# Performance work log

Hardware: AMD Instinct MI355X
Metric: run time of the kernel (lower is better)

Reference implementation:

```python
import jax, jax.numpy as jnp
import numpy as np

OUT = 7          # roi_align output_size
NUM_ANCHORS = 27 # 3 scales x 3 ratios x 3 angles
MAX_PROPOSALS = 100
RPN_STRIDE = 32


def conv2d(x, w, b, stride=1, pad=1):
    y = jax.lax.conv_general_dilated(
        x, w, (stride, stride), [(pad, pad), (pad, pad)],
        dimension_numbers=('NCHW', 'OIHW', 'NCHW'))
    return y + b[None, :, None, None]


def generate_anchors(H, W, stride):
    # matches CustomOrientedRPN.generate_anchors
    sx = np.arange(0, W * stride, stride, dtype=np.float32)
    sy = np.arange(0, H * stride, stride, dtype=np.float32)
    SY, SX = np.meshgrid(sy, sx, indexing='ij')
    shifts = np.stack([SX, SY], axis=-1).reshape(-1, 2)  # [HW,2]
    base = []
    for scale in (32.0, 64.0, 128.0):
        for ratio in (0.5, 1.0, 2.0):
            w = scale * ratio ** 0.5
            h = scale / ratio ** 0.5
            for angle in (0.0, 45.0, 90.0):
                base.append([w, h, angle])
    base = np.array(base, dtype=np.float32)  # [A,3]
    A = base.shape[0]
    anchors = np.concatenate(
        [np.repeat(shifts[:, None, :], A, axis=1),
         np.broadcast_to(base[None], (shifts.shape[0], A, 3))], axis=-1)
    return jnp.asarray(anchors.reshape(-1, 5))  # [HW*A, 5]


def rotated_roi_align(features, boxes, batch_idx):
    # Vectorized version of the per-box affine_grid + grid_sample loop
    # (align_corners=False semantics for both, zero padding for grid_sample).
    B, C, Hf, Wf = features.shape
    lin = (2.0 * jnp.arange(OUT, dtype=features.dtype) + 1.0) / OUT - 1.0
    ys, xs = jnp.meshgrid(lin, lin, indexing='ij')  # [7,7] base grid

    cx, cy, w, h, ang = (boxes[:, i] for i in range(5))
    ar = -ang * jnp.pi / 180.0
    c, s = jnp.cos(ar), jnp.sin(ar)
    t00 = w / Wf * c; t01 = -h / Hf * s; t02 = 2.0 * cx / Wf - 1.0
    t10 = w / Wf * s; t11 = h / Hf * c;  t12 = 2.0 * cy / Hf - 1.0
    gx = t00[:, None, None] * xs + t01[:, None, None] * ys + t02[:, None, None]  # [N,7,7]
    gy = t10[:, None, None] * xs + t11[:, None, None] * ys + t12[:, None, None]

    ix = ((gx + 1.0) * Wf - 1.0) / 2.0
    iy = ((gy + 1.0) * Hf - 1.0) / 2.0
    x0 = jnp.floor(ix); y0 = jnp.floor(iy)
    wx = ix - x0;       wy = iy - y0
    x0i = x0.astype(jnp.int32); y0i = y0.astype(jnp.int32)

    def gather(dx, dy, wgt):
        xi = x0i + dx; yi = y0i + dy
        valid = (xi >= 0) & (xi < Wf) & (yi >= 0) & (yi < Hf)
        xc = jnp.clip(xi, 0, Wf - 1)
        yc = jnp.clip(yi, 0, Hf - 1)
        def one(bi, yb, xb):
            return features[bi][:, yb, xb]  # [C,7,7]
        vals = jax.vmap(one)(batch_idx, yc, xc)  # [N,C,7,7]
        return vals * (wgt * valid)[:, None, :, :]

    return (gather(0, 0, (1 - wx) * (1 - wy)) + gather(1, 0, wx * (1 - wy)) +
            gather(0, 1, (1 - wx) * wy) + gather(1, 1, wx * wy))


def setup_inputs() -> dict:
    key = jax.random.key(0)
    ks = jax.random.split(key, 20)

    def w(k, shape):
        fan_in = int(np.prod(shape[1:]))
        return jax.random.normal(k, shape, jnp.float32) / np.sqrt(fan_in)

    C = 256; A = NUM_ANCHORS; NC = 5
    return {
        'images': jax.random.normal(ks[0], (8, 3, 1024, 1024), jnp.float32),
        'backbone_w': w(ks[1], (C, 3, 3, 3)),   'backbone_b': jnp.zeros((C,), jnp.float32),
        'rpn_conv_w': w(ks[2], (256, C, 3, 3)), 'rpn_conv_b': jnp.zeros((256,), jnp.float32),
        'obj_w': w(ks[3], (A, 256, 1, 1)),      'obj_b': jnp.zeros((A,), jnp.float32),
        'delta_w': w(ks[4], (A * 5, 256, 1, 1)) * 0.1, 'delta_b': jnp.zeros((A * 5,), jnp.float32),
        'fc1_w': w(ks[5], (1024, C * OUT * OUT)), 'fc1_b': jnp.zeros((1024,), jnp.float32),
        'fc2_w': w(ks[6], (1024, 1024)),          'fc2_b': jnp.zeros((1024,), jnp.float32),
        'cls_w': w(ks[7], (NC, 1024)),            'cls_b': jnp.zeros((NC,), jnp.float32),
        'bbox_w': w(ks[8], (5, 1024)),            'bbox_b': jnp.zeros((5,), jnp.float32),
    }


def reference(images, backbone_w, backbone_b, rpn_conv_w, rpn_conv_b,
              obj_w, obj_b, delta_w, delta_b,
              fc1_w, fc1_b, fc2_w, fc2_b, cls_w, cls_b, bbox_w, bbox_b):
    # backbone (stand-in: single stride-16 conv)
    f = conv2d(images, backbone_w, backbone_b, stride=16, pad=1)  # [B,256,64,64]
    B, C, H, W = f.shape
    # F.interpolate(scale_factor=0.5, bilinear, align_corners=False) == 2x2 mean
    f = f.reshape(B, C, H // 2, 2, W // 2, 2).mean(axis=(3, 5))   # [B,256,32,32]
    Hf, Wf = f.shape[2], f.shape[3]

    # RPN
    t = jax.nn.relu(conv2d(f, rpn_conv_w, rpn_conv_b, 1, 1))
    _logits = conv2d(t, obj_w, obj_b, 1, 0)  # computed as in original (unused downstream)
    deltas = conv2d(t, delta_w, delta_b, 1, 0)  # [B, A*5, Hf, Wf]
    A = NUM_ANCHORS
    deltas = deltas.reshape(B, A, 5, Hf, Wf).transpose(0, 3, 4, 1, 2).reshape(B, -1, 5)

    anchors = generate_anchors(Hf, Wf, RPN_STRIDE)  # [HW*A,5]
    acx, acy, aw, ah, aa = (anchors[:, i] for i in range(5))
    pcx = deltas[:, :, 0] * aw + acx
    pcy = deltas[:, :, 1] * ah + acy
    pw = jnp.exp(deltas[:, :, 2]) * aw
    ph = jnp.exp(deltas[:, :, 3]) * ah
    pa = aa + deltas[:, :, 4]
    proposals = jnp.stack([pcx, pcy, pw, ph, pa], axis=-1)  # [B, HW*A, 5]
    proposals = proposals[:, :MAX_PROPOSALS]                # p[:max_proposals]

    boxes = proposals.reshape(-1, 5)                        # [B*100, 5]
    batch_idx = jnp.repeat(jnp.arange(B), MAX_PROPOSALS)
    pooled = rotated_roi_align(f, boxes, batch_idx)         # [B*100, 256, 7, 7]

    x = pooled.reshape(pooled.shape[0], -1)
    x = jax.nn.relu(x @ fc1_w.T + fc1_b)
    x = jax.nn.relu(x @ fc2_w.T + fc2_b)
    class_logits = x @ cls_w.T + cls_b
    obb_preds = x @ bbox_w.T + bbox_b
    return class_logits, obb_preds
```

## Files before the change

### kernel.cpp

```cpp
#include <hip/hip_runtime.h>
#include <hip/hip_bf16.h>

using bf16 = __hip_bfloat16;

typedef __attribute__((ext_vector_type(8))) short bf16x8;
typedef __attribute__((ext_vector_type(4))) float f32x4;

__device__ __forceinline__ void async16(const void* g, void* l) {
  __builtin_amdgcn_global_load_lds(
      (const __attribute__((address_space(1))) unsigned int*)g,
      (__attribute__((address_space(3))) unsigned int*)l, 16, 0, 0);
}

__device__ __forceinline__ void store_o(float* C, size_t i, float v) { C[i] = v; }
__device__ __forceinline__ void store_o(bf16* C, size_t i, float v) {
  C[i] = __float2bfloat16(v);
}

__global__ __launch_bounds__(256) void k_backbone(const float* __restrict__ img,
    const float* __restrict__ w, const float* __restrict__ bias,
    float* __restrict__ f) {
  int blk = blockIdx.x;
  int x = blk & 31, y = (blk >> 5) & 31, b = blk >> 10;
  __shared__ float patch[4 * 27];
  int t = threadIdx.x;
  if (t < 108) {
    int kx = t % 3, ky = (t / 3) % 3, cin = (t / 9) % 3, sub = t / 27;
    int sy = sub >> 1, sx = sub & 1;
    int iy = (2 * y + sy) * 16 - 1 + ky;
    int ix = (2 * x + sx) * 16 - 1 + kx;
    float v = 0.f;
    if (iy >= 0 && ix >= 0)
      v = img[((size_t)(b * 3 + cin) * 1024 + iy) * 1024 + ix];
    patch[t] = v;
  }
  __syncthreads();
  int c = t;
  float wr[27];
#pragma unroll
  for (int k = 0; k < 27; ++k) wr[k] = w[c * 27 + k];
  float acc = 0.f;
#pragma unroll
  for (int sub = 0; sub < 4; ++sub)
#pragma unroll
    for (int k = 0; k < 27; ++k)
      acc += patch[sub * 27 + k] * wr[k];
  f[(size_t)blk * 256 + c] = acc * 0.25f + bias[c];
}

__global__ __launch_bounds__(256) void k_rpn(const float* __restrict__ f,
    const float* __restrict__ rpn_w, float* __restrict__ part) {
  int p = blockIdx.x;
  int kc = blockIdx.y;
  int x = p & 3, b = p >> 2;
  __shared__ float fpl[6][16];
  int tid = threadIdx.x;
  if (tid < 96) {
    int cin2 = tid & 15;
    int rc = tid >> 4;
    int row = rc / 3, col = rc % 3;
    int xc = x - 1 + col;
    float v = 0.f;
    if (xc >= 0)
      v = f[((size_t)(b * 32 + row) * 32 + xc) * 256 + kc * 16 + cin2];
    fpl[rc][cin2] = v;
  }
  __syncthreads();
  int c = tid;
  const float* wbase = rpn_w + (size_t)c * 2304 + kc * 144;
  float acc = 0.f;
#pragma unroll
  for (int cin2 = 0; cin2 < 16; ++cin2) {
    const float* wp = wbase + cin2 * 9;
    acc += fpl[0][cin2] * wp[3] + fpl[1][cin2] * wp[4]
         + fpl[2][cin2] * wp[5] + fpl[3][cin2] * wp[6]
         + fpl[4][cin2] * wp[7] + fpl[5][cin2] * wp[8];
  }
  part[((size_t)kc * 32 + p) * 256 + c] = acc;
}

__global__ __launch_bounds__(512) void k_delta(const float* __restrict__ part,
    const float* __restrict__ rpn_b,
    const float* __restrict__ dw, const float* __restrict__ db,
    float* __restrict__ boxes) {
  int p = blockIdx.x;
  int x = p & 3, b = p >> 2;
  __shared__ float tbuf[256];
  __shared__ float dvals[135];
  int tid = threadIdx.x;
  if (tid < 256) {
    float s = rpn_b[tid];
#pragma unroll
    for (int kc = 0; kc < 16; ++kc)
      s += part[((size_t)kc * 32 + p) * 256 + tid];
    tbuf[tid] = fmaxf(s, 0.f);
  }
  __syncthreads();
  if (tid < 270) {
    int o = tid >> 1, half = tid & 1;
    const float* wp = dw + (size_t)o * 256 + half * 128;
    const float* tp = tbuf + half * 128;
    float s = 0.f;
#pragma unroll 8
    for (int k = 0; k < 128; ++k) s += tp[k] * wp[k];
    s += __shfl_xor(s, 1, 64);
    if (half == 0) dvals[o] = s + db[o];
  }
  __syncthreads();
  if (tid < 27) {
    int i = x * 27 + tid;
    if (i < 100) {
      int a = tid;
      int si = a / 9, ri = (a / 3) % 3, ai = a % 3;
      float scale = 32.f * (float)(1 << si);
      float sr = (ri == 0) ? 0.70710678118654752f : (ri == 1 ? 1.0f : 1.41421356237309505f);
      float aw = scale * sr, ah = scale / sr;
      float aang = 45.f * (float)ai;
      float acx = 32.f * (float)x, acy = 0.f;
      float* bx = boxes + (size_t)(b * 100 + i) * 5;
      bx[0] = dvals[a * 5 + 0] * aw + acx;
      bx[1] = dvals[a * 5 + 1] * ah + acy;
      bx[2] = expf(dvals[a * 5 + 2]) * aw;
      bx[3] = expf(dvals[a * 5 + 3]) * ah;
      bx[4] = aang + dvals[a * 5 + 4];
    }
  }
}

__global__ __launch_bounds__(256) void k_roialign(const float* __restrict__ f,
    const float* __restrict__ boxes, bf16* __restrict__ pooled) {
  int n = blockIdx.x;
  int b = n / 100;
  __shared__ int six[49], siy[49];
  __shared__ float swx[49], swy[49];
  __shared__ float pool_s[12544];
  int tid = threadIdx.x;
  if (tid < 49) {
    float cx = boxes[n * 5 + 0], cy = boxes[n * 5 + 1];
    float w = boxes[n * 5 + 2], h = boxes[n * 5 + 3], ang = boxes[n * 5 + 4];
    float ar = -ang * 0.017453292519943295f;
    float cc = cosf(ar), ss = sinf(ar);
    float t00 = w * (1.f / 32.f) * cc, t01 = -h * (1.f / 32.f) * ss;
    float t02 = cx * (2.f / 32.f) - 1.f;
    float t10 = w * (1.f / 32.f) * ss, t11 = h * (1.f / 32.f) * cc;
    float t12 = cy * (2.f / 32.f) - 1.f;
    int py = tid / 7, px = tid - py * 7;
    float lx = (2.f * px + 1.f) * (1.f / 7.f) - 1.f;
    float ly = (2.f * py + 1.f) * (1.f / 7.f) - 1.f;
    float gx = t00 * lx + t01 * ly + t02;
    float gy = t10 * lx + t11 * ly + t12;
    float ix = ((gx + 1.f) * 32.f - 1.f) * 0.5f;
    float iy = ((gy + 1.f) * 32.f - 1.f) * 0.5f;
    float x0 = floorf(ix), y0 = floorf(iy);
    six[tid] = (int)x0; siy[tid] = (int)y0;
    swx[tid] = ix - x0; swy[tid] = iy - y0;
  }
  __syncthreads();
  const float* fb = f + (size_t)b * 262144;
  int c = tid;
  for (int bin = 0; bin < 49; ++bin) {
    int x0 = six[bin], y0 = siy[bin];
    float wx = swx[bin], wy = swy[bin];
    float acc = 0.f;
    if (x0 >= 0 && x0 < 32 && y0 >= 0 && y0 < 32)
      acc += fb[(y0 * 32 + x0) * 256 + c] * ((1.f - wx) * (1.f - wy));
    if (x0 + 1 >= 0 && x0 + 1 < 32 && y0 >= 0 && y0 < 32)
      acc += fb[(y0 * 32 + x0 + 1) * 256 + c] * (wx * (1.f - wy));
    if (x0 >= 0 && x0 < 32 && y0 + 1 >= 0 && y0 + 1 < 32)
      acc += fb[((y0 + 1) * 32 + x0) * 256 + c] * ((1.f - wx) * wy);
    if (x0 + 1 >= 0 && x0 + 1 < 32 && y0 + 1 >= 0 && y0 + 1 < 32)
      acc += fb[((y0 + 1) * 32 + x0 + 1) * 256 + c] * (wx * wy);
    pool_s[c * 49 + bin] = acc;
  }
  __syncthreads();
  bf16* po = pooled + (size_t)n * 12544;
  for (int k = tid; k < 12544; k += 256) po[k] = __float2bfloat16(pool_s[k]);
}

__global__ __launch_bounds__(256) void k_gemm_sk(
    const unsigned short* __restrict__ A, const float* __restrict__ B,
    float* __restrict__ P, int M, int N, int K, int KC) {
  __shared__ unsigned short As[128 * 64];
  __shared__ unsigned short Bs[64 * 72];
  int t = threadIdx.x;
  int wv = t >> 6, ln = t & 63;
  int quad = ln >> 4, l15 = ln & 15;
  int wm = wv >> 1, wn = wv & 1;
  int n0 = blockIdx.x * 64, m0 = blockIdx.y * 128;
  int kbeg = blockIdx.z * KC;
  int kend = kbeg + KC; if (kend > K) kend = K;

  int srow = ln >> 3;
  int sg = (ln & 7) ^ srow;
  const unsigned short* Ap[4];
#pragma unroll
  for (int q = 0; q < 4; ++q) {
    int r = m0 + q * 32 + wv * 8 + srow;
    if (r > M - 1) r = M - 1;
    Ap[q] = A + (size_t)r * K + sg * 8;
  }

  int brow = t >> 2, bq = t & 3;
  const float* Bp = B + (size_t)(n0 + brow) * K + bq * 16;
  unsigned short* bdst = &Bs[brow * 72 + bq * 16];

  f32x4 acc[4][2];
#pragma unroll
  for (int mf = 0; mf < 4; ++mf)
#pragma unroll
    for (int nf = 0; nf < 2; ++nf) acc[mf][nf] = (f32x4){0.f, 0.f, 0.f, 0.f};

  for (int k0 = kbeg; k0 < kend; k0 += 64) {
    float4 bv0 = *(const float4*)(Bp + k0);
    float4 bv1 = *(const float4*)(Bp + k0 + 4);
    float4 bv2 = *(const float4*)(Bp + k0 + 8);
    float4 bv3 = *(const float4*)(Bp + k0 + 12);
    __syncthreads();
#pragma unroll
    for (int q = 0; q < 4; ++q)
      async16(Ap[q] + k0, &As[q * 2048 + wv * 512]);
    unsigned short bb[16];
    bb[0]  = __bfloat16_as_ushort(__float2bfloat16(bv0.x));
    bb[1]  = __bfloat16_as_ushort(__float2bfloat16(bv0.y));
    bb[2]  = __bfloat16_as_ushort(__float2bfloat16(bv0.z));
    bb[3]  = __bfloat16_as_ushort(__float2bfloat16(bv0.w));
    bb[4]  = __bfloat16_as_ushort(__float2bfloat16(bv1.x));
    bb[5]  = __bfloat16_as_ushort(__float2bfloat16(bv1.y));
    bb[6]  = __bfloat16_as_ushort(__float2bfloat16(bv1.z));
    bb[7]  = __bfloat16_as_ushort(__float2bfloat16(bv1.w));
    bb[8]  = __bfloat16_as_ushort(__float2bfloat16(bv2.x));
    bb[9]  = __bfloat16_as_ushort(__float2bfloat16(bv2.y));
    bb[10] = __bfloat16_as_ushort(__float2bfloat16(bv2.z));
    bb[11] = __bfloat16_as_ushort(__float2bfloat16(bv2.w));
    bb[12] = __bfloat16_as_ushort(__float2bfloat16(bv3.x));
    bb[13] = __bfloat16_as_ushort(__float2bfloat16(bv3.y));
    bb[14] = __bfloat16_as_ushort(__float2bfloat16(bv3.z));
    bb[15] = __bfloat16_as_ushort(__float2bfloat16(bv3.w));
#pragma unroll
    for (int u = 0; u < 2; ++u)
      *(bf16x8*)(bdst + u * 8) = *(const bf16x8*)(bb + u * 8);
    __syncthreads();
#pragma unroll
    for (int ks = 0; ks < 2; ++ks) {
      bf16x8 a[4];
#pragma unroll
      for (int mf = 0; mf < 4; ++mf) {
        int row = wm * 64 + mf * 16 + l15;
        a[mf] = *(const bf16x8*)&As[row * 64 + (((ks * 4 + quad) ^ (l15 & 7)) * 8)];
      }
#pragma unroll
      for (int nf = 0; nf < 2; ++nf) {
        bf16x8 b = *(const bf16x8*)&Bs[(wn * 32 + nf * 16 + l15) * 72 + ks * 32 + quad * 8];
#pragma unroll
        for (int mf = 0; mf < 4; ++mf)
          acc[mf][nf] = __builtin_amdgcn_mfma_f32_16x16x32_bf16(a[mf], b, acc[mf][nf], 0, 0, 0);
      }
    }
  }
#pragma unroll
  for (int nf = 0; nf < 2; ++nf) {
    int n = n0 + wn * 32 + nf * 16 + l15;
#pragma unroll
    for (int mf = 0; mf < 4; ++mf) {
#pragma unroll
      for (int r = 0; r < 4; ++r) {
        int m = m0 + wm * 64 + mf * 16 + quad * 4 + r;
        if (m < M) atomicAdd(&P[(size_t)m * N + n], acc[mf][nf][r]);
      }
    }
  }
}

template <typename OutT>
__global__ __launch_bounds__(256) void k_bias_relu(const float* __restrict__ P,
    const float* __restrict__ bias, OutT* __restrict__ C, int MN, int N) {
  int i = blockIdx.x * 256 + threadIdx.x;
  if (i * 4 >= MN) return;
  f32x4 s = *(const f32x4*)(P + (size_t)i * 4);
  int n = (i * 4) % N;
#pragma unroll
  for (int u = 0; u < 4; ++u)
    store_o(C, (size_t)i * 4 + u, fmaxf(s[u] + bias[n + u], 0.f));
}

__global__ __launch_bounds__(640) void k_heads(const float* __restrict__ x2,
    const float* __restrict__ cls_w, const float* __restrict__ cls_b,
    const float* __restrict__ bbox_w, const float* __restrict__ bbox_b,
    float* __restrict__ out) {
  int n = blockIdx.x;
  int wave = threadIdx.x >> 6;
  int lane = threadIdx.x & 63;
  const float* w = (wave < 5) ? (cls_w + (size_t)wave * 1024)
                              : (bbox_w + (size_t)(wave - 5) * 1024);
  const float* xr = x2 + (size_t)n * 1024;
  float s = 0.f;
  for (int k = lane; k < 1024; k += 64) s += xr[k] * w[k];
  for (int off = 32; off; off >>= 1) s += __shfl_down(s, off, 64);
  if (lane == 0) {
    int o = (wave < 5) ? wave : wave - 5;
    float bias = (wave < 5) ? cls_b[o] : bbox_b[o];
    int base = (wave < 5) ? 0 : 4000;
    out[base + n * 5 + o] = s + bias;
  }
}

extern "C" void kernel_launch(void* const* d_in, const int* in_sizes, int n_in,
                              void* d_out, int out_size, void* d_ws, size_t ws_size,
                              hipStream_t stream) {
  const float* images     = (const float*)d_in[0];
  const float* backbone_w = (const float*)d_in[1];
  const float* backbone_b = (const float*)d_in[2];
  const float* rpn_w      = (const float*)d_in[3];
  const float* rpn_b      = (const float*)d_in[4];
  const float* delta_w    = (const float*)d_in[7];
  const float* delta_b    = (const float*)d_in[8];
  const float* fc1_w      = (const float*)d_in[9];
  const float* fc1_b      = (const float*)d_in[10];
  const float* fc2_w      = (const float*)d_in[11];
  const float* fc2_b      = (const float*)d_in[12];
  const float* cls_w      = (const float*)d_in[13];
  const float* cls_b      = (const float*)d_in[14];
  const float* bbox_w     = (const float*)d_in[15];
  const float* bbox_b     = (const float*)d_in[16];

  char* ws = (char*)d_ws;
  float* f      = (float*)ws;
  float* boxes  = (float*)(ws + 8388608);
  bf16*  pooled = (bf16*) (ws + 8404992);
  bf16*  x1     = (bf16*) (ws + 28475392);
  float* x2     = (float*)(ws + 30113792);
  float* P      = (float*)(ws + 33390592);
  float* rpart = P;

  k_backbone<<<8192, 256, 0, stream>>>(images, backbone_w, backbone_b, f);
  k_rpn<<<dim3(32, 16), 256, 0, stream>>>(f, rpn_w, rpart);
  k_delta<<<32, 512, 0, stream>>>(rpart, rpn_b, delta_w, delta_b, boxes);
  k_roialign<<<800, 256, 0, stream>>>(f, boxes, pooled);

  hipMemsetAsync(P, 0, 3276800, stream);
  k_gemm_sk<<<dim3(16, 7, 12), 256, 0, stream>>>(
      (const unsigned short*)pooled, fc1_w, P, 800, 1024, 12544, 1088);
  k_bias_relu<bf16><<<800, 256, 0, stream>>>(P, fc1_b, x1, 819200, 1024);

  hipMemsetAsync(P, 0, 3276800, stream);
  k_gemm_sk<<<dim3(16, 7, 8), 256, 0, stream>>>(
      (const unsigned short*)x1, fc2_w, P, 800, 1024, 1024, 128);
  k_bias_relu<float><<<800, 256, 0, stream>>>(P, fc2_b, x2, 819200, 1024);

  k_heads<<<800, 640, 0, stream>>>(x2, cls_w, cls_b, bbox_w, bbox_b, (float*)d_out);
}
```

Before: 359.1 us.

## Pre-convert FC weights to bf16 and widen GEMM N-tile with async B loads

Adds a conversion kernel that casts fc1/fc2 weights from fp32 to bf16 into workspace on every call. The GEMM now loads B through async global-to-LDS copies with the same swizzle as A, and each block covers 128 columns instead of 64. This removes the per-tile fp32 load and convert work from the inner loop and halves how often the A tile is re-read. In exchange it adds a full extra pass over the 51MB fp32 fc1 weight, plus a reshuffled workspace layout that aliases the weight buffer with the backbone features and pooled with x2.

After: 374.0 us. +4.2%, slower.

```diff
diff --git a/kernel.cpp b/kernel.cpp
--- a/kernel.cpp
+++ b/kernel.cpp
@@ -177,16 +177,33 @@
   for (int k = tid; k < 12544; k += 256) po[k] = __float2bfloat16(pool_s[k]);
 }
 
-__global__ __launch_bounds__(256) void k_gemm_sk(
-    const unsigned short* __restrict__ A, const float* __restrict__ B,
+__device__ __forceinline__ unsigned int pk2(float a, float b) {
+  unsigned int ua = __bfloat16_as_ushort(__float2bfloat16(a));
+  unsigned int ub = __bfloat16_as_ushort(__float2bfloat16(b));
+  return ua | (ub << 16);
+}
+__global__ __launch_bounds__(256) void k_cvt(const float* __restrict__ s,
+    uint2* __restrict__ d, int n4) {
+  int stride = gridDim.x * 256;
+  for (int j = blockIdx.x * 256 + threadIdx.x; j < n4; j += stride) {
+    float4 v = ((const float4*)s)[j];
+    uint2 o;
+    o.x = pk2(v.x, v.y);
+    o.y = pk2(v.z, v.w);
+    d[j] = o;
+  }
+}
+
+__global__ __launch_bounds__(256) void k_gemm_bb(
+    const unsigned short* __restrict__ A, const unsigned short* __restrict__ B,
     float* __restrict__ P, int M, int N, int K, int KC) {
   __shared__ unsigned short As[128 * 64];
-  __shared__ unsigned short Bs[64 * 72];
+  __shared__ unsigned short Bs[128 * 64];
   int t = threadIdx.x;
   int wv = t >> 6, ln = t & 63;
   int quad = ln >> 4, l15 = ln & 15;
   int wm = wv >> 1, wn = wv & 1;
-  int n0 = blockIdx.x * 64, m0 = blockIdx.y * 128;
+  int n0 = blockIdx.x * 128, m0 = blockIdx.y * 128;
   int kbeg = blockIdx.z * KC;
   int kend = kbeg + KC; if (kend > K) kend = K;
 
@@ -199,46 +216,27 @@
     if (r > M - 1) r = M - 1;
     Ap[q] = A + (size_t)r * K + sg * 8;
   }
-
-  int brow = t >> 2, bq = t & 3;
-  const float* Bp = B + (size_t)(n0 + brow) * K + bq * 16;
-  unsigned short* bdst = &Bs[brow * 72 + bq * 16];
-
-  f32x4 acc[4][2];
+  const unsigned short* Bp[4];
+#pragma unroll
+  for (int c = 0; c < 4; ++c) {
+    int r = n0 + wv * 32 + c * 8 + srow;
+    Bp[c] = B + (size_t)r * K + sg * 8;
+  }
+
+  f32x4 acc[4][4];
 #pragma unroll
   for (int mf = 0; mf < 4; ++mf)
 #pragma unroll
-    for (int nf = 0; nf < 2; ++nf) acc[mf][nf] = (f32x4){0.f, 0.f, 0.f, 0.f};
+    for (int nf = 0; nf < 4; ++nf) acc[mf][nf] = (f32x4){0.f, 0.f, 0.f, 0.f};
 
   for (int k0 = kbeg; k0 < kend; k0 += 64) {
-    float4 bv0 = *(const float4*)(Bp + k0);
-    float4 bv1 = *(const float4*)(Bp + k0 + 4);
-    float4 bv2 = *(const float4*)(Bp + k0 + 8);
-    float4 bv3 = *(const float4*)(Bp + k0 + 12);
     __syncthreads();
 #pragma unroll
     for (int q = 0; q < 4; ++q)
       async16(Ap[q] + k0, &As[q * 2048 + wv * 512]);
-    unsigned short bb[16];
-    bb[0]  = __bfloat16_as_ushort(__float2bfloat16(bv0.x));
-    bb[1]  = __bfloat16_as_ushort(__float2bfloat16(bv0.y));
-    bb[2]  = __bfloat16_as_ushort(__float2bfloat16(bv0.z));
-    bb[3]  = __bfloat16_as_ushort(__float2bfloat16(bv0.w));
-    bb[4]  = __bfloat16_as_ushort(__float2bfloat16(bv1.x));
-    bb[5]  = __bfloat16_as_ushort(__float2bfloat16(bv1.y));
-    bb[6]  = __bfloat16_as_ushort(__float2bfloat16(bv1.z));
-    bb[7]  = __bfloat16_as_ushort(__float2bfloat16(bv1.w));
-    bb[8]  = __bfloat16_as_ushort(__float2bfloat16(bv2.x));
-    bb[9]  = __bfloat16_as_ushort(__float2bfloat16(bv2.y));
-    bb[10] = __bfloat16_as_ushort(__float2bfloat16(bv2.z));
-    bb[11] = __bfloat16_as_ushort(__float2bfloat16(bv2.w));
-    bb[12] = __bfloat16_as_ushort(__float2bfloat16(bv3.x));
-    bb[13] = __bfloat16_as_ushort(__float2bfloat16(bv3.y));
-    bb[14] = __bfloat16_as_ushort(__float2bfloat16(bv3.z));
-    bb[15] = __bfloat16_as_ushort(__float2bfloat16(bv3.w));
-#pragma unroll
-    for (int u = 0; u < 2; ++u)
-      *(bf16x8*)(bdst + u * 8) = *(const bf16x8*)(bb + u * 8);
+#pragma unroll
+    for (int c = 0; c < 4; ++c)
+      async16(Bp[c] + k0, &Bs[wv * 2048 + c * 512]);
     __syncthreads();
 #pragma unroll
     for (int ks = 0; ks < 2; ++ks) {
@@ -249,8 +247,9 @@
         a[mf] = *(const bf16x8*)&As[row * 64 + (((ks * 4 + quad) ^ (l15 & 7)) * 8)];
       }
 #pragma unroll
-      for (int nf = 0; nf < 2; ++nf) {
-        bf16x8 b = *(const bf16x8*)&Bs[(wn * 32 + nf * 16 + l15) * 72 + ks * 32 + quad * 8];
+      for (int nf = 0; nf < 4; ++nf) {
+        int brow = wn * 64 + nf * 16 + l15;
+        bf16x8 b = *(const bf16x8*)&Bs[brow * 64 + (((ks * 4 + quad) ^ (l15 & 7)) * 8)];
 #pragma unroll
         for (int mf = 0; mf < 4; ++mf)
           acc[mf][nf] = __builtin_amdgcn_mfma_f32_16x16x32_bf16(a[mf], b, acc[mf][nf], 0, 0, 0);
@@ -258,8 +257,8 @@
     }
   }
 #pragma unroll
-  for (int nf = 0; nf < 2; ++nf) {
-    int n = n0 + wn * 32 + nf * 16 + l15;
+  for (int nf = 0; nf < 4; ++nf) {
+    int n = n0 + wn * 64 + nf * 16 + l15;
 #pragma unroll
     for (int mf = 0; mf < 4; ++mf) {
 #pragma unroll
@@ -324,27 +323,34 @@
   const float* bbox_b     = (const float*)d_in[16];
 
   char* ws = (char*)d_ws;
+  bf16*  bw1    = (bf16*) ws;
   float* f      = (float*)ws;
-  float* boxes  = (float*)(ws + 8388608);
-  bf16*  pooled = (bf16*) (ws + 8404992);
-  bf16*  x1     = (bf16*) (ws + 28475392);
-  float* x2     = (float*)(ws + 30113792);
-  float* P      = (float*)(ws + 33390592);
-  float* rpart = P;
+  float* boxes  = (float*)(ws + 25690112);
+  bf16*  pooled = (bf16*) (ws + 25706496);
+  float* x2     = (float*)(ws + 25706496);
+  bf16*  x1     = (bf16*) (ws + 45776896);
+  float* P      = (float*)(ws + 47415296);
+  bf16*  bw2    = (bf16*) (ws + 50692096);
+  float* rpart  = P;
 
   k_backbone<<<8192, 256, 0, stream>>>(images, backbone_w, backbone_b, f);
   k_rpn<<<dim3(32, 16), 256, 0, stream>>>(f, rpn_w, rpart);
   k_delta<<<32, 512, 0, stream>>>(rpart, rpn_b, delta_w, delta_b, boxes);
   k_roialign<<<800, 256, 0, stream>>>(f, boxes, pooled);
 
+  k_cvt<<<2048, 256, 0, stream>>>(fc1_w, (uint2*)bw1, 3211264);
+  k_cvt<<<512, 256, 0, stream>>>(fc2_w, (uint2*)bw2, 262144);
+
   hipMemsetAsync(P, 0, 3276800, stream);
-  k_gemm_sk<<<dim3(16, 7, 12), 256, 0, stream>>>(
-      (const unsigned short*)pooled, fc1_w, P, 800, 1024, 12544, 1088);
+  k_gemm_bb<<<dim3(8, 7, 12), 256, 0, stream>>>(
+      (const unsigned short*)pooled, (const unsigned short*)bw1, P,
+      800, 1024, 12544, 1088);
   k_bias_relu<bf16><<<800, 256, 0, stream>>>(P, fc1_b, x1, 819200, 1024);
 
   hipMemsetAsync(P, 0, 3276800, stream);
-  k_gemm_sk<<<dim3(16, 7, 8), 256, 0, stream>>>(
-      (const unsigned short*)x1, fc2_w, P, 800, 1024, 1024, 128);
+  k_gemm_bb<<<dim3(8, 7, 8), 256, 0, stream>>>(
+      (const unsigned short*)x1, (const unsigned short*)bw2, P,
+      800, 1024, 1024, 128);
   k_bias_relu<float><<<800, 256, 0, stream>>>(P, fc2_b, x2, 819200, 1024);
 
   k_heads<<<800, 640, 0, stream>>>(x2, cls_w, cls_b, bbox_w, bbox_b, (float*)d_out);
```
